# Kernel optimization log

Measured on AMD Instinct MI355X. Metric: run time of the kernel, lower is better.

Reference implementation:

```python
import jax, jax.numpy as jnp
import numpy as np

B, C, H, W, OC, K = 8, 256, 120, 120, 256, 3


def setup_inputs() -> dict:
    key = jax.random.key(0)
    ks = jax.random.split(key, 6)
    x = jax.random.normal(ks[0], (B, C, H, W), jnp.float32)
    y = jax.random.normal(ks[1], (B, C, H, W), jnp.float32)
    # generate_kernel: 1x1 conv in_yC -> in_xC (weight stored as (out, in))
    gen_w = jax.random.normal(ks[2], (C, C), jnp.float32) * (1.0 / np.sqrt(C))
    gen_b = jax.random.normal(ks[3], (C,), jnp.float32) * 0.01
    # fuse: 3x3 conv in_xC -> out_C, padding 1
    fuse_w = jax.random.normal(ks[4], (OC, C, 3, 3), jnp.float32) * (1.0 / np.sqrt(C * 9))
    fuse_b = jax.random.normal(ks[5], (OC,), jnp.float32) * 0.01
    return {"x": x, "y": y, "gen_w": gen_w, "gen_b": gen_b,
            "fuse_w": fuse_w, "fuse_b": fuse_b}


def reference(x, y, gen_w, gen_b, fuse_w, fuse_b):
    b, c, h, w = x.shape
    # AdaptiveAvgPool2d(K): H,W divisible by K -> uniform average pooling
    yp = y.reshape(b, c, K, h // K, K, w // K).mean(axis=(3, 5))  # (B,C,K,K)
    # 1x1 conv to generate per-sample per-channel kernels
    kernel = jnp.einsum('oc,bcij->boij', gen_w, yp) + gen_b[None, :, None, None]
    # dynamic depthwise conv: groups = B*C, padding 1 (cross-correlation, as torch)
    xg = x.reshape(1, b * c, h, w)
    kg = kernel.reshape(b * c, 1, K, K)
    dn = jax.lax.conv_dimension_numbers(xg.shape, kg.shape, ('NCHW', 'OIHW', 'NCHW'))
    out = jax.lax.conv_general_dilated(
        xg, kg, window_strides=(1, 1), padding=((1, 1), (1, 1)),
        dimension_numbers=dn, feature_group_count=b * c)
    out = out.reshape(b, c, h, w)
    # fuse: dense 3x3 conv C -> OC, padding 1, with bias
    dn2 = jax.lax.conv_dimension_numbers(out.shape, fuse_w.shape, ('NCHW', 'OIHW', 'NCHW'))
    res = jax.lax.conv_general_dilated(
        out, fuse_w, window_strides=(1, 1), padding=((1, 1), (1, 1)),
        dimension_numbers=dn2)
    return res + fuse_b[None, :, None, None]
```

## Files before the change

kernel.cpp:

```cpp
#include <hip/hip_runtime.h>
#include <hip/hip_bf16.h>
#include <stdint.h>

#define TB 8
#define TC 256
#define TH 120
#define TW 120
#define THW 14400
#define TOC 256
#define PH 122
#define PW 122

typedef short bf16x8 __attribute__((ext_vector_type(8)));
typedef float f32x4 __attribute__((ext_vector_type(4)));

#define OUTP_BYTES ((size_t)TB * PH * PW * TC * 2)
#define YP_OFF     OUTP_BYTES
#define DK_OFF     (YP_OFF + (size_t)TB * TC * 9 * 4)
#define WP_OFF     (DK_OFF + (size_t)TB * TC * 9 * 4)

__global__ void zero_halo_kernel(char* __restrict__ outP) {
    int i = blockIdx.x * 256 + threadIdx.x;
    int pos_idx = i >> 5, part = i & 31;
    int b = pos_idx / 484; int k = pos_idx - b * 484;
    int h, w;
    if (k < 122)      { h = 0;   w = k; }
    else if (k < 244) { h = 121; w = k - 122; }
    else { int m = k - 244; h = 1 + (m >> 1); w = (m & 1) ? 121 : 0; }
    size_t pos = ((size_t)b * PH + h) * PW + w;
    uint4 z; z.x = 0u; z.y = 0u; z.z = 0u; z.w = 0u;
    *(uint4*)(outP + pos * 512 + part * 16) = z;
}

__global__ __launch_bounds__(128) void pool_kernel(const float* __restrict__ y,
                                                   float* __restrict__ yp) {
    int bc = blockIdx.x, t = threadIdx.x;
    __shared__ float pr[120][4];
    __shared__ float p2[9][8];
    const float* src = y + (size_t)bc * THW;
    if (t < 120) {
        const float4* row = (const float4*)(src + t * TW);
        float s0 = 0.f, s1 = 0.f, s2 = 0.f;
        #pragma unroll
        for (int j = 0; j < 10; ++j)  { float4 v = row[j]; s0 += (v.x + v.y) + (v.z + v.w); }
        #pragma unroll
        for (int j = 10; j < 20; ++j) { float4 v = row[j]; s1 += (v.x + v.y) + (v.z + v.w); }
        #pragma unroll
        for (int j = 20; j < 30; ++j) { float4 v = row[j]; s2 += (v.x + v.y) + (v.z + v.w); }
        pr[t][0] = s0; pr[t][1] = s1; pr[t][2] = s2;
    }
    __syncthreads();
    if (t < 72) {
        int bin = t >> 3, ch = t & 7;
        int bh = bin / 3, bw = bin - bh * 3;
        float a = 0.f;
        #pragma unroll
        for (int r = 0; r < 5; ++r) a += pr[bh * 40 + ch * 5 + r][bw];
        p2[bin][ch] = a;
    }
    __syncthreads();
    if (t < 9) {
        float a = 0.f;
        #pragma unroll
        for (int j = 0; j < 8; ++j) a += p2[t][j];
        yp[bc * 9 + t] = a * (1.f / 1600.f);
    }
}

__global__ void gen_kernel(const float* __restrict__ yp, const float* __restrict__ gen_w,
                           const float* __restrict__ gen_b, float* __restrict__ dk) {
    int b = blockIdx.x, t = threadIdx.x;
    __shared__ float yps[TC * 9];
    for (int i = t; i < TC * 9; i += 256) yps[i] = yp[b * TC * 9 + i];
    __syncthreads();
    float acc[9];
    float bias = gen_b[t];
    #pragma unroll
    for (int j = 0; j < 9; ++j) acc[j] = bias;
    for (int c = 0; c < TC; ++c) {
        float w = gen_w[t * TC + c];
        #pragma unroll
        for (int j = 0; j < 9; ++j) acc[j] += w * yps[c * 9 + j];
    }
    #pragma unroll
    for (int j = 0; j < 9; ++j) dk[(b * TC + t) * 9 + j] = acc[j];
}

__global__ __launch_bounds__(1024) void dw_kernel(const float* __restrict__ x,
        const float* __restrict__ dk, __hip_bfloat16* __restrict__ outP) {
    int bid = blockIdx.x;
    int hs = bid & 7;
    int cc = (bid >> 3) & 7;
    int b  = bid >> 6;
    int t = threadIdx.x;
    int c  = t >> 5;
    int wq = t & 31;
    bool active = wq < 30;
    int w0 = wq * 4;
    int cg = cc * 32 + c;
    const float* xp = x + (size_t)(b * TC + cg) * THW;
    const float* dkp = dk + (size_t)(b * TC + cg) * 9;
    float k0[3], k1[3], k2[3];
    #pragma unroll
    for (int j = 0; j < 3; ++j) { k0[j] = dkp[j]; k1[j] = dkp[3 + j]; k2[j] = dkp[6 + j]; }

    __shared__ __align__(16) __hip_bfloat16 stage[2][32][124];

    int h0 = hs * 15;
    float A[6], B[6], C[6];
    auto loadrow = [&](int hh, float* V) {
        if (hh < 0 || hh >= TH) {
            #pragma unroll
            for (int j = 0; j < 6; ++j) V[j] = 0.f;
            return;
        }
        const float* row = xp + hh * TW;
        float4 v = *(const float4*)(row + w0);
        V[1] = v.x; V[2] = v.y; V[3] = v.z; V[4] = v.w;
        V[0] = (wq > 0)  ? row[w0 - 1] : 0.f;
        V[5] = (wq < 29) ? row[w0 + 4] : 0.f;
    };
    if (active) { loadrow(h0 - 1, A); loadrow(h0, B); }

    for (int r = 0; r < 15; ++r) {
        int h = h0 + r;
        if (active) {
            loadrow(h + 1, C);
            ushort4 pk;
            #pragma unroll
            for (int i = 0; i < 4; ++i) {
                float o = A[i] * k0[0] + A[i + 1] * k0[1] + A[i + 2] * k0[2]
                        + B[i] * k1[0] + B[i + 1] * k1[1] + B[i + 2] * k1[2]
                        + C[i] * k2[0] + C[i + 1] * k2[1] + C[i + 2] * k2[2];
                __hip_bfloat16 hb = __float2bfloat16(o);
                ushort u = *(ushort*)&hb;
                if (i == 0) pk.x = u; else if (i == 1) pk.y = u;
                else if (i == 2) pk.z = u; else pk.w = u;
            }
            *(ushort4*)&stage[r & 1][c][w0] = pk;
            #pragma unroll
            for (int j = 0; j < 6; ++j) { A[j] = B[j]; B[j] = C[j]; }
        }
        __syncthreads();
        if (t < 480) {
            int w = t >> 2, part = t & 3;
            ushort vals[8];
            #pragma unroll
            for (int j = 0; j < 8; ++j) vals[j] = *(const ushort*)&stage[r & 1][part * 8 + j][w];
            uint4 o;
            o.x = (uint)vals[0] | ((uint)vals[1] << 16);
            o.y = (uint)vals[2] | ((uint)vals[3] << 16);
            o.z = (uint)vals[4] | ((uint)vals[5] << 16);
            o.w = (uint)vals[6] | ((uint)vals[7] << 16);
            size_t pos = ((size_t)b * PH + (h + 1)) * PW + (w + 1);
            *(uint4*)((char*)outP + pos * 512 + cc * 64 + part * 16) = o;
        }
    }
}

__global__ void wprep_kernel(const float* __restrict__ fuse_w, __hip_bfloat16* __restrict__ Wp) {
    int i = blockIdx.x * 256 + threadIdx.x;
    int ij = i >> 16;
    int oc = (i >> 8) & 255;
    int c  = i & 255;
    Wp[i] = __float2bfloat16(fuse_w[(oc * 256 + c) * 9 + ij]);
}

typedef const __attribute__((address_space(1))) char* gas_t;
typedef __attribute__((address_space(3))) char* las_t;
__device__ __forceinline__ void gload16(const char* g, char* l) {
    __builtin_amdgcn_global_load_lds((gas_t)g, (las_t)l, 16, 0, 0);
}

__global__ __launch_bounds__(256, 2) void gemm_kernel(
        const __hip_bfloat16* __restrict__ outP,
        const __hip_bfloat16* __restrict__ Wp,
        const float* __restrict__ fuse_b,
        float* __restrict__ res) {
    __shared__ __align__(16) char lds[2][32768];
    const int t = threadIdx.x;
    const int lane = t & 63;
    const int wv = t >> 6;
    const int wo = wv >> 1;
    const int wm = wv & 1;

    const int bid0 = blockIdx.x;
    const int logical = (bid0 & 7) * 225 + (bid0 >> 3);
    const int bn = logical & 1;
    const int bm = logical >> 1;

    const char* gI = (const char*)outP;
    const char* gW = (const char*)Wp;

    const int rbp = (((lane & 7) ^ (lane >> 3)) << 4);
    int srcI[4], srcW[4];
    #pragma unroll
    for (int q = 0; q < 4; ++q) {
        int p = (q * 4 + wv) * 8 + (lane >> 3);
        int m = bm * 128 + p;
        int b = m / THW; int r = m - b * THW;
        int h = r / TW;  int w = r - h * TW;
        srcI[q] = (((b * PH + h) * PW + w) << 9) + rbp;
        srcW[q] = ((bn * 128 + p) << 9) + rbp;
    }
    const int segBase = wv * 1024;

    int aWb[4], aWs[4], aIb[4], aIs[4];
    #pragma unroll
    for (int i = 0; i < 4; ++i) {
        int rw = wo * 64 + i * 16 + (lane & 15);
        aWb[i] = rw * 128; aWs[i] = (rw & 7) << 4;
        int ri = wm * 64 + i * 16 + (lane & 15);
        aIb[i] = ri * 128; aIs[i] = (ri & 7) << 4;
    }
    const int klo = (lane >> 4) << 4;

    f32x4 acc[4][4];
    #pragma unroll
    for (int i = 0; i < 4; ++i) {
        #pragma unroll
        for (int j = 0; j < 4; ++j) {
            f32x4 z = {0.f, 0.f, 0.f, 0.f};
            acc[i][j] = z;
        }
    }

    auto step_offs = [&](int s, int& offI, int& offW) {
        int ij = s >> 2;
        int c0b = (s & 3) << 7;
        int di = ij / 3, dj = ij - (ij / 3) * 3;
        offI = ((di * PW + dj) << 9) + c0b;
        offW = (ij << 17) + c0b;
    };
    auto STAGE = [&](int buf, int s) {
        int offI, offW; step_offs(s, offI, offW);
        char* LI = &lds[buf][0];
        char* LW = &lds[buf][16384];
        #pragma unroll
        for (int q = 0; q < 4; ++q) {
            gload16(gI + srcI[q] + offI, LI + segBase + q * 4096);
            gload16(gW + srcW[q] + offW, LW + segBase + q * 4096);
        }
    };
    auto COMPUTE = [&](int buf) {
        const char* LI = &lds[buf][0];
        const char* LW = &lds[buf][16384];
        #pragma unroll
        for (int kk = 0; kk < 2; ++kk) {
            int ck = kk * 64 + klo;
            bf16x8 wf[4], iff[4];
            #pragma unroll
            for (int i = 0; i < 4; ++i)
                wf[i] = *(const bf16x8*)(LW + aWb[i] + (ck ^ aWs[i]));
            #pragma unroll
            for (int i = 0; i < 4; ++i)
                iff[i] = *(const bf16x8*)(LI + aIb[i] + (ck ^ aIs[i]));
            __builtin_amdgcn_s_setprio(1);
            #pragma unroll
            for (int o = 0; o < 4; ++o) {
                #pragma unroll
                for (int mi = 0; mi < 4; ++mi)
                    acc[o][mi] = __builtin_amdgcn_mfma_f32_16x16x32_bf16(
                        wf[o], iff[mi], acc[o][mi], 0, 0, 0);
            }
            __builtin_amdgcn_s_setprio(0);
        }
    };

    STAGE(0, 0);
    #pragma unroll 1
    for (int s = 0; s < 35; ++s) {
        int cur = s & 1;
        STAGE(cur ^ 1, s + 1);
        asm volatile("s_waitcnt vmcnt(8)" ::: "memory");
        __builtin_amdgcn_s_barrier();
        asm volatile("" ::: "memory");
        COMPUTE(cur);
        asm volatile("" ::: "memory");
        __builtin_amdgcn_s_barrier();
        asm volatile("" ::: "memory");
    }
    asm volatile("s_waitcnt vmcnt(0)" ::: "memory");
    __builtin_amdgcn_s_barrier();
    asm volatile("" ::: "memory");
    COMPUTE(1);

    int baseM[4];
    #pragma unroll
    for (int mt = 0; mt < 4; ++mt) {
        int m = bm * 128 + wm * 64 + mt * 16 + (lane & 15);
        int b = m / THW; int r = m - b * THW;
        baseM[mt] = b * (TOC * THW) + r;
    }
    const int ocb0 = bn * 128 + wo * 64 + ((lane >> 4) << 2);
    float bias[4][4];
    #pragma unroll
    for (int o = 0; o < 4; ++o) {
        #pragma unroll
        for (int g = 0; g < 4; ++g)
            bias[o][g] = fuse_b[ocb0 + o * 16 + g];
    }
    #pragma unroll
    for (int o = 0; o < 4; ++o) {
        #pragma unroll
        for (int mt = 0; mt < 4; ++mt) {
            #pragma unroll
            for (int g = 0; g < 4; ++g)
                res[baseM[mt] + (ocb0 + o * 16 + g) * THW] = acc[o][mt][g] + bias[o][g];
        }
    }
}

extern "C" void kernel_launch(void* const* d_in, const int* in_sizes, int n_in,
                              void* d_out, int out_size, void* d_ws, size_t ws_size,
                              hipStream_t stream) {
    const float* x      = (const float*)d_in[0];
    const float* y      = (const float*)d_in[1];
    const float* gen_w  = (const float*)d_in[2];
    const float* gen_b  = (const float*)d_in[3];
    const float* fuse_w = (const float*)d_in[4];
    const float* fuse_b = (const float*)d_in[5];
    float* out = (float*)d_out;
    char* ws = (char*)d_ws;

    __hip_bfloat16* outP = (__hip_bfloat16*)(ws);
    float* yp = (float*)(ws + YP_OFF);
    float* dk = (float*)(ws + DK_OFF);
    __hip_bfloat16* Wp = (__hip_bfloat16*)(ws + WP_OFF);

    zero_halo_kernel<<<484, 256, 0, stream>>>((char*)outP);
    pool_kernel<<<TB * TC, 128, 0, stream>>>(y, yp);
    gen_kernel<<<TB, 256, 0, stream>>>(yp, gen_w, gen_b, dk);
    wprep_kernel<<<2304, 256, 0, stream>>>(fuse_w, Wp);
    dw_kernel<<<512, 1024, 0, stream>>>(x, dk, outP);
    gemm_kernel<<<1800, 256, 0, stream>>>(outP, Wp, fuse_b, out);
}
```

Baseline: 243.7 us.

## Enlarge GEMM tile to 256x256 with 8 waves and interleaved LDS pipeline

The implicit-GEMM 3x3 conv kernel now computes a 256-row by 256-column output tile per block with 512 threads (8 waves, each 128x64), instead of 128x128 tiles with 4 waves. The main loop is restructured into a ping-pong schedule that interleaves half-tile global-to-LDS loads, LDS fragment reads and MFMA quarters separated by barriers. The goal is to raise arithmetic intensity and cut redundant reloads of the input and weight tiles. In exchange it uses 128KB of LDS per block and only 450 blocks, which may limit occupancy and leave the grid with a partial final wave across CUs.

```diff
diff --git a/kernel.cpp b/kernel.cpp
--- a/kernel.cpp
+++ b/kernel.cpp
@@ -171,142 +171,165 @@
 __device__ __forceinline__ void gload16(const char* g, char* l) {
     __builtin_amdgcn_global_load_lds((gas_t)g, (las_t)l, 16, 0, 0);
 }
-
-__global__ __launch_bounds__(256, 2) void gemm_kernel(
+__device__ __forceinline__ void barrier_() {
+    asm volatile("" ::: "memory");
+    __builtin_amdgcn_s_barrier();
+    asm volatile("" ::: "memory");
+}
+
+__global__ __launch_bounds__(512, 2) void gemm_kernel(
         const __hip_bfloat16* __restrict__ outP,
         const __hip_bfloat16* __restrict__ Wp,
         const float* __restrict__ fuse_b,
         float* __restrict__ res) {
-    __shared__ __align__(16) char lds[2][32768];
+    __shared__ __align__(16) char lds[2][65536];
     const int t = threadIdx.x;
     const int lane = t & 63;
     const int wv = t >> 6;
-    const int wo = wv >> 1;
-    const int wm = wv & 1;
-
-    const int bid0 = blockIdx.x;
-    const int logical = (bid0 & 7) * 225 + (bid0 >> 3);
-    const int bn = logical & 1;
-    const int bm = logical >> 1;
+    const int wm = wv >> 2;
+    const int wn = wv & 3;
+    const int bm = blockIdx.x;
 
     const char* gI = (const char*)outP;
     const char* gW = (const char*)Wp;
 
-    const int rbp = (((lane & 7) ^ (lane >> 3)) << 4);
-    int srcI[4], srcW[4];
-    #pragma unroll
-    for (int q = 0; q < 4; ++q) {
-        int p = (q * 4 + wv) * 8 + (lane >> 3);
-        int m = bm * 128 + p;
-        int b = m / THW; int r = m - b * THW;
-        int h = r / TW;  int w = r - h * TW;
-        srcI[q] = (((b * PH + h) * PW + w) << 9) + rbp;
-        srcW[q] = ((bn * 128 + p) << 9) + rbp;
-    }
-    const int segBase = wv * 1024;
-
-    int aWb[4], aWs[4], aIb[4], aIs[4];
-    #pragma unroll
-    for (int i = 0; i < 4; ++i) {
-        int rw = wo * 64 + i * 16 + (lane & 15);
-        aWb[i] = rw * 128; aWs[i] = (rw & 7) << 4;
-        int ri = wm * 64 + i * 16 + (lane & 15);
-        aIb[i] = ri * 128; aIs[i] = (ri & 7) << 4;
-    }
+    const int sw  = (lane & 7) << 4;
     const int klo = (lane >> 4) << 4;
-
-    f32x4 acc[4][4];
-    #pragma unroll
-    for (int i = 0; i < 4; ++i) {
-        #pragma unroll
-        for (int j = 0; j < 4; ++j) {
-            f32x4 z = {0.f, 0.f, 0.f, 0.f};
-            acc[i][j] = z;
-        }
-    }
-
-    auto step_offs = [&](int s, int& offI, int& offW) {
-        int ij = s >> 2;
-        int c0b = (s & 3) << 7;
-        int di = ij / 3, dj = ij - (ij / 3) * 3;
-        offI = ((di * PW + dj) << 9) + c0b;
-        offW = (ij << 17) + c0b;
-    };
-    auto STAGE = [&](int buf, int s) {
-        int offI, offW; step_offs(s, offI, offW);
-        char* LI = &lds[buf][0];
-        char* LW = &lds[buf][16384];
-        #pragma unroll
-        for (int q = 0; q < 4; ++q) {
-            gload16(gI + srcI[q] + offI, LI + segBase + q * 4096);
-            gload16(gW + srcW[q] + offW, LW + segBase + q * 4096);
-        }
-    };
-    auto COMPUTE = [&](int buf) {
-        const char* LI = &lds[buf][0];
-        const char* LW = &lds[buf][16384];
-        #pragma unroll
-        for (int kk = 0; kk < 2; ++kk) {
-            int ck = kk * 64 + klo;
-            bf16x8 wf[4], iff[4];
-            #pragma unroll
-            for (int i = 0; i < 4; ++i)
-                wf[i] = *(const bf16x8*)(LW + aWb[i] + (ck ^ aWs[i]));
-            #pragma unroll
-            for (int i = 0; i < 4; ++i)
-                iff[i] = *(const bf16x8*)(LI + aIb[i] + (ck ^ aIs[i]));
-            __builtin_amdgcn_s_setprio(1);
-            #pragma unroll
-            for (int o = 0; o < 4; ++o) {
-                #pragma unroll
-                for (int mi = 0; mi < 4; ++mi)
-                    acc[o][mi] = __builtin_amdgcn_mfma_f32_16x16x32_bf16(
-                        wf[o], iff[mi], acc[o][mi], 0, 0, 0);
-            }
-            __builtin_amdgcn_s_setprio(0);
-        }
-    };
-
-    STAGE(0, 0);
+    const int rowA0 = wm * 128 + (lane & 15);
+    const int aA_k0 = rowA0 * 128 + (klo ^ sw);
+    const int aA_k1 = rowA0 * 128 + ((64 + klo) ^ sw);
+    const int rowB0 = wn * 64 + (lane & 15);
+    const int aB_k0 = 32768 + rowB0 * 128 + (klo ^ sw);
+    const int aB_k1 = 32768 + rowB0 * 128 + ((64 + klo) ^ sw);
+
+    const int srb = (((lane & 7) ^ (lane >> 3)) << 4);
+    int srcA[2][2], srcB[2][2];
+    #pragma unroll
+    for (int h = 0; h < 2; ++h) {
+        #pragma unroll
+        for (int r = 0; r < 2; ++r) {
+            int p = r * 64 + wv * 8 + (lane >> 3);
+            int m = bm * 256 + h * 128 + p;
+            int b = m / THW; int rr = m - b * THW;
+            int hh = rr / TW; int w = rr - hh * TW;
+            srcA[h][r] = (((b * PH + hh) * PW + w) << 9) + srb;
+            srcB[h][r] = ((h * 128 + p) << 9) + srb;
+        }
+    }
+
+    bf16x8 rA[8], rB[8];
+    f32x4 acc[8][4];
+    #pragma unroll
+    for (int f = 0; f < 8; ++f) {
+        #pragma unroll
+        for (int g = 0; g < 4; ++g) { f32x4 z = {0.f,0.f,0.f,0.f}; acc[f][g] = z; }
+    }
+
+    auto OFFI = [&](int s) {
+        int ij = s >> 2; int di = ij / 3, dj = ij - di * 3;
+        return ((di * PW + dj) << 9) + ((s & 3) << 7);
+    };
+    auto OFFW = [&](int s) {
+        return ((s >> 2) << 17) + ((s & 3) << 7);
+    };
+    auto STA = [&](int buf, int h, int offI) {
+        char* base = &lds[buf][h * 16384 + t * 16];
+        gload16(gI + srcA[h][0] + offI, base);
+        gload16(gI + srcA[h][1] + offI, base + 8192);
+    };
+    auto STB = [&](int buf, int h, int offW) {
+        char* base = &lds[buf][32768 + h * 16384 + t * 16];
+        gload16(gW + srcB[h][0] + offW, base);
+        gload16(gW + srcB[h][1] + offW, base + 8192);
+    };
+
+#define DS_A(BUF, MH) \
+    { _Pragma("unroll") for (int f = 0; f < 4; ++f) { \
+        rA[f*2+0] = *(const bf16x8*)(&lds[BUF][0] + aA_k0 + (MH)*8192 + f*2048); \
+        rA[f*2+1] = *(const bf16x8*)(&lds[BUF][0] + aA_k1 + (MH)*8192 + f*2048); } }
+#define DS_B(BUF, OH) \
+    { _Pragma("unroll") for (int g = 0; g < 2; ++g) { \
+        rB[(OH)*4+g*2+0] = *(const bf16x8*)(&lds[BUF][0] + aB_k0 + (OH)*4096 + g*2048); \
+        rB[(OH)*4+g*2+1] = *(const bf16x8*)(&lds[BUF][0] + aB_k1 + (OH)*4096 + g*2048); } }
+#define MMA(MH, OH) \
+    { __builtin_amdgcn_s_setprio(1); \
+      _Pragma("unroll") for (int kk = 0; kk < 2; ++kk) \
+        _Pragma("unroll") for (int f = 0; f < 4; ++f) \
+          _Pragma("unroll") for (int g = 0; g < 2; ++g) \
+            acc[(MH)*4+f][(OH)*2+g] = __builtin_amdgcn_mfma_f32_16x16x32_bf16( \
+                rB[(OH)*4+g*2+kk], rA[f*2+kk], acc[(MH)*4+f][(OH)*2+g], 0, 0, 0); \
+      __builtin_amdgcn_s_setprio(0); }
+
+    {
+        int offI0 = OFFI(0), offW0 = OFFW(0), offW1 = OFFW(1);
+        STA(0, 0, offI0); STA(0, 1, offI0);
+        STB(0, 0, offW0); STB(0, 1, offW0);
+        STB(1, 0, offW1); STB(1, 1, offW1);
+    }
+    asm volatile("s_waitcnt vmcnt(4)" ::: "memory");
+    barrier_();
+
     #pragma unroll 1
-    for (int s = 0; s < 35; ++s) {
-        int cur = s & 1;
-        STAGE(cur ^ 1, s + 1);
-        asm volatile("s_waitcnt vmcnt(8)" ::: "memory");
-        __builtin_amdgcn_s_barrier();
-        asm volatile("" ::: "memory");
-        COMPUTE(cur);
-        asm volatile("" ::: "memory");
-        __builtin_amdgcn_s_barrier();
-        asm volatile("" ::: "memory");
-    }
-    asm volatile("s_waitcnt vmcnt(0)" ::: "memory");
-    __builtin_amdgcn_s_barrier();
-    asm volatile("" ::: "memory");
-    COMPUTE(1);
-
-    int baseM[4];
-    #pragma unroll
-    for (int mt = 0; mt < 4; ++mt) {
-        int m = bm * 128 + wm * 64 + mt * 16 + (lane & 15);
-        int b = m / THW; int r = m - b * THW;
-        baseM[mt] = b * (TOC * THW) + r;
-    }
-    const int ocb0 = bn * 128 + wo * 64 + ((lane >> 4) << 2);
+    for (int it = 0; it < 18; ++it) {
+        const int t1 = 2 * it + 1, t2 = 2 * it + 2, t3 = 2 * it + 3;
+        const bool has2 = t2 < 36, has3 = t3 < 36;
+        const int offI1 = OFFI(t1);
+        const int offI2 = has2 ? OFFI(t2) : 0;
+        const int offW2 = has2 ? OFFW(t2) : 0;
+        const int offW3 = has3 ? OFFW(t3) : 0;
+
+        DS_A(0, 0); DS_B(0, 0);
+        STA(1, 0, offI1);
+        barrier_(); MMA(0, 0); barrier_();
+        DS_B(0, 1);
+        STA(1, 1, offI1);
+        barrier_(); MMA(0, 1); barrier_();
+        DS_A(0, 1);
+        if (has2) STB(0, 0, offW2);
+        barrier_(); MMA(1, 0); barrier_();
+        if (has2) STB(0, 1, offW2);
+        if (it < 17) { asm volatile("s_waitcnt vmcnt(4)" ::: "memory"); }
+        else         { asm volatile("s_waitcnt vmcnt(0)" ::: "memory"); }
+        barrier_(); MMA(1, 1); barrier_();
+        DS_A(1, 0); DS_B(1, 0);
+        if (has2) STA(0, 0, offI2);
+        barrier_(); MMA(0, 0); barrier_();
+        DS_B(1, 1);
+        if (has2) STA(0, 1, offI2);
+        barrier_(); MMA(0, 1); barrier_();
+        DS_A(1, 1);
+        if (has3) STB(1, 0, offW3);
+        barrier_(); MMA(1, 0); barrier_();
+        if (has3) STB(1, 1, offW3);
+        if (it < 17) { asm volatile("s_waitcnt vmcnt(4)" ::: "memory"); }
+        else         { asm volatile("s_waitcnt vmcnt(0)" ::: "memory"); }
+        barrier_(); MMA(1, 1); barrier_();
+    }
+#undef DS_A
+#undef DS_B
+#undef MMA
+
+    int baseM[8];
+    #pragma unroll
+    for (int f = 0; f < 8; ++f) {
+        int m = bm * 256 + wm * 128 + f * 16 + (lane & 15);
+        int b = m / THW; int rr = m - b * THW;
+        baseM[f] = b * (TOC * THW) + rr;
+    }
+    const int oc0 = wn * 64 + ((lane >> 4) << 2);
     float bias[4][4];
     #pragma unroll
-    for (int o = 0; o < 4; ++o) {
-        #pragma unroll
-        for (int g = 0; g < 4; ++g)
-            bias[o][g] = fuse_b[ocb0 + o * 16 + g];
-    }
-    #pragma unroll
-    for (int o = 0; o < 4; ++o) {
-        #pragma unroll
-        for (int mt = 0; mt < 4; ++mt) {
-            #pragma unroll
-            for (int g = 0; g < 4; ++g)
-                res[baseM[mt] + (ocb0 + o * 16 + g) * THW] = acc[o][mt][g] + bias[o][g];
+    for (int g = 0; g < 4; ++g) {
+        #pragma unroll
+        for (int j = 0; j < 4; ++j) bias[g][j] = fuse_b[oc0 + g * 16 + j];
+    }
+    #pragma unroll
+    for (int g = 0; g < 4; ++g) {
+        #pragma unroll
+        for (int f = 0; f < 8; ++f) {
+            #pragma unroll
+            for (int j = 0; j < 4; ++j)
+                res[baseM[f] + (oc0 + g * 16 + j) * THW] = acc[f][g][j] + bias[g][j];
         }
     }
 }
@@ -333,5 +356,5 @@
     gen_kernel<<<TB, 256, 0, stream>>>(yp, gen_w, gen_b, dk);
     wprep_kernel<<<2304, 256, 0, stream>>>(fuse_w, Wp);
     dw_kernel<<<512, 1024, 0, stream>>>(x, dk, outP);
-    gemm_kernel<<<1800, 256, 0, stream>>>(outP, Wp, fuse_b, out);
-}
+    gemm_kernel<<<450, 512, 0, stream>>>(outP, Wp, fuse_b, out);
+}
```

Result: no change. 247.5 us (+1.6%).

## Split gen_kernel over output-channel groups and batch dw_kernel row flushes

Applied to the files above, without the earlier changes.

gen_kernel now runs 64 blocks instead of 8. Each block handles 32 output channels, splits the input-channel reduction across 8 thread segments and combines them with a shared-memory tree reduction, which adds parallelism to a latency-bound tiny kernel. dw_kernel now computes two rows per iteration into a double-buffered stage and flushes the previous pair using 960 threads. This halves the number of __syncthreads barriers and overlaps the stores with compute. The cost is more shared memory and somewhat more complex indexing.

```diff
diff --git a/kernel.cpp b/kernel.cpp
--- a/kernel.cpp
+++ b/kernel.cpp
@@ -67,23 +67,44 @@
     }
 }
 
-__global__ void gen_kernel(const float* __restrict__ yp, const float* __restrict__ gen_w,
-                           const float* __restrict__ gen_b, float* __restrict__ dk) {
-    int b = blockIdx.x, t = threadIdx.x;
+__global__ __launch_bounds__(256) void gen_kernel(const float* __restrict__ yp,
+        const float* __restrict__ gen_w, const float* __restrict__ gen_b,
+        float* __restrict__ dk) {
+    int blk = blockIdx.x;
+    int b = blk >> 3, ocg = blk & 7;
+    int t = threadIdx.x;
+    int ocl = t & 31, cseg = t >> 5;
+    int oc = ocg * 32 + ocl;
     __shared__ float yps[TC * 9];
     for (int i = t; i < TC * 9; i += 256) yps[i] = yp[b * TC * 9 + i];
     __syncthreads();
     float acc[9];
-    float bias = gen_b[t];
-    #pragma unroll
-    for (int j = 0; j < 9; ++j) acc[j] = bias;
-    for (int c = 0; c < TC; ++c) {
-        float w = gen_w[t * TC + c];
-        #pragma unroll
-        for (int j = 0; j < 9; ++j) acc[j] += w * yps[c * 9 + j];
-    }
-    #pragma unroll
-    for (int j = 0; j < 9; ++j) dk[(b * TC + t) * 9 + j] = acc[j];
+    #pragma unroll
+    for (int j = 0; j < 9; ++j) acc[j] = 0.f;
+    const float* wrow = gen_w + (size_t)oc * TC + cseg * 32;
+    for (int c = 0; c < 32; ++c) {
+        float w = wrow[c];
+        const float* yrow = &yps[(cseg * 32 + c) * 9];
+        #pragma unroll
+        for (int j = 0; j < 9; ++j) acc[j] += w * yrow[j];
+    }
+    __shared__ float red[8][32][9];
+    #pragma unroll
+    for (int j = 0; j < 9; ++j) red[cseg][ocl][j] = acc[j];
+    __syncthreads();
+    for (int st = 4; st > 0; st >>= 1) {
+        if (cseg < st) {
+            #pragma unroll
+            for (int j = 0; j < 9; ++j) red[cseg][ocl][j] += red[cseg + st][ocl][j];
+        }
+        __syncthreads();
+    }
+    if (cseg == 0) {
+        float bias = gen_b[oc];
+        #pragma unroll
+        for (int j = 0; j < 9; ++j)
+            dk[((size_t)b * TC + oc) * 9 + j] = red[0][ocl][j] + bias;
+    }
 }
 
 __global__ __launch_bounds__(1024) void dw_kernel(const float* __restrict__ x,
@@ -104,7 +125,7 @@
     #pragma unroll
     for (int j = 0; j < 3; ++j) { k0[j] = dkp[j]; k1[j] = dkp[3 + j]; k2[j] = dkp[6 + j]; }
 
-    __shared__ __align__(16) __hip_bfloat16 stage[2][32][124];
+    __shared__ __align__(16) __hip_bfloat16 stage[2][2][32][124];
 
     int h0 = hs * 15;
     float A[6], B[6], C[6];
@@ -120,42 +141,54 @@
         V[0] = (wq > 0)  ? row[w0 - 1] : 0.f;
         V[5] = (wq < 29) ? row[w0 + 4] : 0.f;
     };
+    auto comp = [&](int r, int par, int sub) {
+        if (!active) return;
+        loadrow(h0 + r + 1, C);
+        ushort4 pk;
+        #pragma unroll
+        for (int i = 0; i < 4; ++i) {
+            float o = A[i] * k0[0] + A[i + 1] * k0[1] + A[i + 2] * k0[2]
+                    + B[i] * k1[0] + B[i + 1] * k1[1] + B[i + 2] * k1[2]
+                    + C[i] * k2[0] + C[i + 1] * k2[1] + C[i + 2] * k2[2];
+            __hip_bfloat16 hb = __float2bfloat16(o);
+            ushort u = *(ushort*)&hb;
+            if (i == 0) pk.x = u; else if (i == 1) pk.y = u;
+            else if (i == 2) pk.z = u; else pk.w = u;
+        }
+        *(ushort4*)&stage[par][sub][c][w0] = pk;
+        #pragma unroll
+        for (int j = 0; j < 6; ++j) { A[j] = B[j]; B[j] = C[j]; }
+    };
+    auto flushrow = [&](int r, int par, int sub, int tt) {
+        int w = tt >> 2, part = tt & 3;
+        ushort vals[8];
+        #pragma unroll
+        for (int j = 0; j < 8; ++j) vals[j] = *(const ushort*)&stage[par][sub][part * 8 + j][w];
+        uint4 o;
+        o.x = (uint)vals[0] | ((uint)vals[1] << 16);
+        o.y = (uint)vals[2] | ((uint)vals[3] << 16);
+        o.z = (uint)vals[4] | ((uint)vals[5] << 16);
+        o.w = (uint)vals[6] | ((uint)vals[7] << 16);
+        size_t pos = ((size_t)b * PH + (h0 + r + 1)) * PW + (w + 1);
+        *(uint4*)((char*)outP + pos * 512 + cc * 64 + part * 16) = o;
+    };
+
     if (active) { loadrow(h0 - 1, A); loadrow(h0, B); }
-
-    for (int r = 0; r < 15; ++r) {
-        int h = h0 + r;
-        if (active) {
-            loadrow(h + 1, C);
-            ushort4 pk;
-            #pragma unroll
-            for (int i = 0; i < 4; ++i) {
-                float o = A[i] * k0[0] + A[i + 1] * k0[1] + A[i + 2] * k0[2]
-                        + B[i] * k1[0] + B[i + 1] * k1[1] + B[i + 2] * k1[2]
-                        + C[i] * k2[0] + C[i + 1] * k2[1] + C[i + 2] * k2[2];
-                __hip_bfloat16 hb = __float2bfloat16(o);
-                ushort u = *(ushort*)&hb;
-                if (i == 0) pk.x = u; else if (i == 1) pk.y = u;
-                else if (i == 2) pk.z = u; else pk.w = u;
-            }
-            *(ushort4*)&stage[r & 1][c][w0] = pk;
-            #pragma unroll
-            for (int j = 0; j < 6; ++j) { A[j] = B[j]; B[j] = C[j]; }
+    comp(0, 0, 0); comp(1, 0, 1);
+    __syncthreads();
+    #pragma unroll 1
+    for (int p = 1; p < 8; ++p) {
+        int r0 = 2 * p;
+        comp(r0, p & 1, 0);
+        if (r0 + 1 < 15) comp(r0 + 1, p & 1, 1);
+        if (t < 960) {
+            int fr = t >= 480 ? 1 : 0;
+            int tt = t - fr * 480;
+            flushrow(2 * (p - 1) + fr, (p - 1) & 1, fr, tt);
         }
         __syncthreads();
-        if (t < 480) {
-            int w = t >> 2, part = t & 3;
-            ushort vals[8];
-            #pragma unroll
-            for (int j = 0; j < 8; ++j) vals[j] = *(const ushort*)&stage[r & 1][part * 8 + j][w];
-            uint4 o;
-            o.x = (uint)vals[0] | ((uint)vals[1] << 16);
-            o.y = (uint)vals[2] | ((uint)vals[3] << 16);
-            o.z = (uint)vals[4] | ((uint)vals[5] << 16);
-            o.w = (uint)vals[6] | ((uint)vals[7] << 16);
-            size_t pos = ((size_t)b * PH + (h + 1)) * PW + (w + 1);
-            *(uint4*)((char*)outP + pos * 512 + cc * 64 + part * 16) = o;
-        }
-    }
+    }
+    if (t < 480) flushrow(14, 1, 0, t);
 }
 
 __global__ void wprep_kernel(const float* __restrict__ fuse_w, __hip_bfloat16* __restrict__ Wp) {
@@ -330,7 +363,7 @@
 
     zero_halo_kernel<<<484, 256, 0, stream>>>((char*)outP);
     pool_kernel<<<TB * TC, 128, 0, stream>>>(y, yp);
-    gen_kernel<<<TB, 256, 0, stream>>>(yp, gen_w, gen_b, dk);
+    gen_kernel<<<64, 256, 0, stream>>>(yp, gen_w, gen_b, dk);
     wprep_kernel<<<2304, 256, 0, stream>>>(fuse_w, Wp);
     dw_kernel<<<512, 1024, 0, stream>>>(x, dk, outP);
     gemm_kernel<<<1800, 256, 0, stream>>>(outP, Wp, fuse_b, out);
```

Measured after the change: 223.9 us. 1.09x faster.
